# Kernel optimization log

Measured on AMD Instinct MI355X. Metric: run time of the kernel, lower is better.

## Reference

```python
import jax, jax.numpy as jnp
import numpy as np

N = 50000      # nodes
E = 800000     # edges (avg degree 16)
IN = 64        # in_channels
H = 128        # hidden_channels
OUT = 64       # out_channels
NS = 10        # n_samples
EPS = 1e-5     # BatchNorm eps


def _sage_conv(x, src, dst, Wl, bl, Wr):
    # PyG SAGEConv (mean aggr): lin_l(mean_neighbors) + lin_r(x)
    n = x.shape[0]
    deg = jax.ops.segment_sum(jnp.ones(src.shape[0], x.dtype), dst, num_segments=n)
    agg = jax.ops.segment_sum(x[src], dst, num_segments=n) / jnp.clip(deg, 1.0)[:, None]
    return agg @ Wl + bl + x @ Wr


def _batchnorm(x, gamma, beta):
    # training-mode BN forward (batch statistics), deterministic
    m = x.mean(axis=0)
    v = x.var(axis=0)
    return (x - m) * jax.lax.rsqrt(v + EPS) * gamma + beta


def setup_inputs() -> dict:
    key = jax.random.key(0)
    ks = jax.random.split(key, 40)
    w = lambda k, shape: (jax.random.normal(k, shape, jnp.float32) * 0.05)
    inp = {
        "x": jax.random.normal(ks[0], (N, IN), jnp.float32),
        "edge_index": jax.random.randint(ks[1], (2, E), 0, N, dtype=jnp.int32),
        "batch": jnp.zeros((N,), jnp.int32),
        "noise": jax.random.normal(ks[2], (NS, N, OUT), jnp.float32),
        # encoder1: SAGEConv(IN,H) + BN(H)
        "We1l": w(ks[3], (IN, H)), "be1": jnp.zeros((H,), jnp.float32), "We1r": w(ks[4], (IN, H)),
        "g1": jnp.ones((H,), jnp.float32), "b1": jnp.zeros((H,), jnp.float32),
        # encoder2: SAGEConv(H,2H) + BN(2H) + SAGEConv(2H,2*OUT)
        "We2l": w(ks[5], (H, 2 * H)), "be2": jnp.zeros((2 * H,), jnp.float32), "We2r": w(ks[6], (H, 2 * H)),
        "g2": jnp.ones((2 * H,), jnp.float32), "b2": jnp.zeros((2 * H,), jnp.float32),
        "We3l": w(ks[7], (2 * H, 2 * OUT)), "be3": jnp.zeros((2 * OUT,), jnp.float32), "We3r": w(ks[8], (2 * H, 2 * OUT)),
        # x1_transform: Linear(H, IN)
        "Wt": w(ks[9], (H, IN)), "bt": jnp.zeros((IN,), jnp.float32),
        # decoder1: Linear(OUT+IN, H) + BN(H); decoder2: Linear(H, IN)
        "Wd1": w(ks[10], (OUT + IN, H)), "bd1": jnp.zeros((H,), jnp.float32),
        "gd": jnp.ones((H,), jnp.float32), "bd": jnp.zeros((H,), jnp.float32),
        "Wd2": w(ks[11], (H, IN)), "bd2": jnp.zeros((IN,), jnp.float32),
        # SAGPooling score GNN = GraphConv(H, 1): lin_rel (bias) + lin_root (no bias)
        "Wp_rel": w(ks[12], (H, 1)), "bp": jnp.zeros((1,), jnp.float32), "Wp_root": w(ks[13], (H, 1)),
    }
    return inp


def reference(x, edge_index, batch, noise,
              We1l, be1, We1r, g1, b1,
              We2l, be2, We2r, g2, b2,
              We3l, be3, We3r,
              Wt, bt, Wd1, bd1, gd, bd, Wd2, bd2,
              Wp_rel, bp, Wp_root):
    src, dst = edge_index[0], edge_index[1]

    # ---- encode ----
    x1 = _batchnorm(jax.nn.relu(_sage_conv(x, src, dst, We1l, be1, We1r)), g1, b1)
    x2 = _batchnorm(jax.nn.relu(_sage_conv(x1, src, dst, We2l, be2, We2r)), g2, b2)
    ms = _sage_conv(x2, src, dst, We3l, be3, We3r)        # [N, 2*OUT]
    mean, log_std = ms[:, :OUT], ms[:, OUT:]

    # ---- reparameterize: avg of n_samples draws == mean + std * mean(eps) ----
    z = mean + jnp.exp(log_std) * noise.mean(axis=0)

    # ---- decode ----
    x1t = x1 @ Wt + bt                                    # [N, IN]
    h = jax.nn.relu(jnp.concatenate([z, x1t], axis=-1) @ Wd1 + bd1)
    h = _batchnorm(h, gd, bd)
    reconstruction = h @ Wd2 + bd2                        # [N, IN]

    # ---- SAGPooling (ratio=0.5) on x1 ----
    agg = jax.ops.segment_sum(x1[src], dst, num_segments=N)   # GraphConv add-aggr
    score = jnp.tanh((agg @ Wp_rel + bp + x1 @ Wp_root)[:, 0])  # [N]
    k = N // 2
    _, perm = jax.lax.top_k(score, k)                     # kept node indices (desc score)

    keep = jnp.zeros((N,), bool).at[perm].set(True)
    newidx = jnp.zeros((N,), jnp.int32).at[perm].set(jnp.arange(k, dtype=jnp.int32))
    edge_mask = keep[src] & keep[dst]                     # edges surviving the pooling
    ei_cg = newidx[edge_index]                            # [2, E], valid where edge_mask
    # unpool: map coarse indices back to original node ids; -1 marks dropped edges
    edge_index_unpooled = jnp.where(edge_mask[None, :], perm[ei_cg].astype(jnp.int32), -1)
    x_unpooled = x1[perm]                                 # [k, H]

    return (reconstruction, x_unpooled, edge_index_unpooled, edge_mask, mean, log_std, x1)
```

## Files before the change

### kernel.cpp

```cpp
#include <hip/hip_runtime.h>
#include <hip/hip_bf16.h>
#include <math.h>

#define NN 50000
#define EE 800000
#define KHALF 25000
#define NSAMP 2048
#define NBK (NSAMP+1)

typedef short bf16x8 __attribute__((ext_vector_type(8)));
typedef short sh4 __attribute__((ext_vector_type(4)));
typedef float f32x4 __attribute__((ext_vector_type(4)));

static __device__ inline unsigned short f2bf(float f){
  __hip_bfloat16 h = __float2bfloat16(f);
  return __builtin_bit_cast(unsigned short, h);
}
static __device__ inline float bf2f(unsigned short u){
  unsigned int x = ((unsigned int)u)<<16;
  return __builtin_bit_cast(float, x);
}

__global__ void k_hist(const int* __restrict__ dst, int* __restrict__ cnt, int E){
  int i = blockIdx.x*blockDim.x + threadIdx.x;
  if(i<E) atomicAdd(&cnt[dst[i]], 1);
}

__global__ void k_scan(const int* __restrict__ deg, int* __restrict__ rowptr, int n){
  __shared__ int sm[1024];
  int t = threadIdx.x;
  int chunk = (n + 1023) >> 10;
  int b = t*chunk; int e = b+chunk; if(b>n) b=n; if(e>n) e=n;
  int s=0;
  for(int i=b;i<e;i++) s += deg[i];
  sm[t]=s; __syncthreads();
  for(int off=1; off<1024; off<<=1){
    int add = (t>=off)? sm[t-off] : 0;
    __syncthreads();
    sm[t] += add;
    __syncthreads();
  }
  int run = sm[t]-s;
  for(int i=b;i<e;i++){ rowptr[i]=run; run += deg[i]; }
  if(t==1023) rowptr[n]=sm[1023];
}

__global__ void k_fill(const int* __restrict__ src, const int* __restrict__ dst,
                       const int* __restrict__ rowptr, int* __restrict__ cnt,
                       int* __restrict__ csr, int E){
  int i = blockIdx.x*blockDim.x + threadIdx.x;
  if(i<E){
    int d = dst[i];
    int p = rowptr[d] + atomicAdd(&cnt[d],1);
    csr[p] = src[i];
  }
}

template<typename AccT, typename OT, int F, int VW>
__global__ void k_segmean(const float* __restrict__ x, const int* __restrict__ csr,
                          const int* __restrict__ rowptr, OT* __restrict__ out, int n){
  int gid = blockIdx.x*blockDim.x + threadIdx.x;
  int node = gid >> 6; int lane = gid & 63;
  if(node>=n) return;
  int b = rowptr[node], e = rowptr[node+1];
  AccT acc[VW];
  #pragma unroll
  for(int k=0;k<VW;k++) acc[k]=(AccT)0;
  const float* xp = x + lane*VW;
  for(int j=b;j<e;j++){
    const float* row = xp + (long)csr[j]*F;
    if(VW==1){
      acc[0] += (AccT)row[0];
    } else if(VW==2){
      float2 v = *(const float2*)row;
      acc[0]+=(AccT)v.x; acc[1]+=(AccT)v.y;
    } else {
      float4 v = *(const float4*)row;
      acc[0]+=(AccT)v.x; acc[1]+=(AccT)v.y; acc[2]+=(AccT)v.z; acc[3]+=(AccT)v.w;
    }
  }
  int d = e-b; if(d<1) d=1;
  AccT inv = (AccT)1 / (AccT)d;
  #pragma unroll
  for(int k=0;k<VW;k++) out[(long)node*F + lane*VW + k] = (OT)(acc[k]*inv);
}

__global__ void k_segmean_ms(const float* __restrict__ T3, const float* __restrict__ msr,
                             const int* __restrict__ csr, const int* __restrict__ rowptr,
                             float* __restrict__ omean, float* __restrict__ olstd, int n){
  int gid = blockIdx.x*blockDim.x + threadIdx.x;
  int node = gid >> 6; int lane = gid & 63;
  if(node>=n) return;
  int b = rowptr[node], e = rowptr[node+1];
  float a0=0.f, a1=0.f;
  const float* xp = T3 + lane*2;
  for(int j=b;j<e;j++){
    float2 v = *(const float2*)(xp + (long)csr[j]*128);
    a0+=v.x; a1+=v.y;
  }
  int d=e-b; if(d<1)d=1;
  float inv = 1.f/(float)d;
  float2 mv = *(const float2*)(msr + (long)node*128 + lane*2);
  float2 r; r.x = a0*inv + mv.x; r.y = a1*inv + mv.y;
  int c0 = lane*2;
  if(c0 < 64) *(float2*)(omean + (long)node*64 + c0)      = r;
  else        *(float2*)(olstd + (long)node*64 + (c0-64)) = r;
}

__global__ __launch_bounds__(256) void k_gemm_bf16s(
    const float* __restrict__ A, const float* __restrict__ W1, int K1,
    const float* __restrict__ X, const float* __restrict__ W2, int K2,
    const float* __restrict__ bias, float* __restrict__ out,
    int M, int J, int relu)
{
  __shared__ __align__(16) short Ah[128*64];
  __shared__ __align__(16) short Al[128*64];
  __shared__ __align__(16) short Bh[64*64];
  __shared__ __align__(16) short Bl[64*64];
  const int m0 = blockIdx.x*128, n0 = blockIdx.y*64;
  const int t = threadIdx.x;
  const int lane = t & 63, wid = t >> 6;
  const int wm = wid >> 1, wn = wid & 1;

  f32x4 acc[4][2];
  #pragma unroll
  for(int i=0;i<4;i++)
    #pragma unroll
    for(int j=0;j<2;j++) acc[i][j] = (f32x4){0.f,0.f,0.f,0.f};

  const int ns1 = K1 >> 6;
  const int ns2 = X ? (K2 >> 6) : 0;
  for(int s=0; s<ns1+ns2; ++s){
    const float* P; const float* W; int K, k0;
    if(s < ns1){ P = A; W = W1; K = K1; k0 = s*64; }
    else       { P = X; W = W2; K = K2; k0 = (s-ns1)*64; }

    #pragma unroll
    for(int i=0;i<8;i++){
      int f4  = t + i*256;
      int row = f4 >> 4, c4 = f4 & 15;
      int gr  = m0 + row;
      float4 v = make_float4(0.f,0.f,0.f,0.f);
      if(gr < M) v = *(const float4*)(P + (long)gr*K + k0 + c4*4);
      unsigned short h0=f2bf(v.x), h1=f2bf(v.y), h2=f2bf(v.z), h3=f2bf(v.w);
      sh4 hi = (sh4){(short)h0,(short)h1,(short)h2,(short)h3};
      sh4 lo = (sh4){(short)f2bf(v.x-bf2f(h0)), (short)f2bf(v.y-bf2f(h1)),
                     (short)f2bf(v.z-bf2f(h2)), (short)f2bf(v.w-bf2f(h3))};
      int byte = (row*128 + c4*8) ^ ((row&7)<<4);
      *(sh4*)((char*)Ah + byte) = hi;
      *(sh4*)((char*)Al + byte) = lo;
    }
    {
      int n = t & 63, k4 = (t>>6)<<2;
      #pragma unroll
      for(int i=0;i<4;i++){
        int kb = i*16 + k4;
        const float* wp = W + (long)(k0+kb)*J + n0 + n;
        float w0 = wp[0], w1 = wp[J], w2 = wp[2*J], w3 = wp[3*J];
        unsigned short h0=f2bf(w0), h1=f2bf(w1), h2=f2bf(w2), h3=f2bf(w3);
        sh4 hi = (sh4){(short)h0,(short)h1,(short)h2,(short)h3};
        sh4 lo = (sh4){(short)f2bf(w0-bf2f(h0)), (short)f2bf(w1-bf2f(h1)),
                       (short)f2bf(w2-bf2f(h2)), (short)f2bf(w3-bf2f(h3))};
        int byte = (n*128 + kb*2) ^ ((n&7)<<4);
        *(sh4*)((char*)Bh + byte) = hi;
        *(sh4*)((char*)Bl + byte) = lo;
      }
    }
    __syncthreads();

    #pragma unroll
    for(int kk=0;kk<2;kk++){
      int kb = kk*32 + (lane>>4)*8;
      bf16x8 ahf[4], alf[4], bhf[2], blf[2];
      #pragma unroll
      for(int mf=0; mf<4; mf++){
        int r = wm*64 + mf*16 + (lane&15);
        int byte = (r*128 + kb*2) ^ ((r&7)<<4);
        ahf[mf] = *(const bf16x8*)((const char*)Ah + byte);
        alf[mf] = *(const bf16x8*)((const char*)Al + byte);
      }
      #pragma unroll
      for(int nf=0; nf<2; nf++){
        int n = wn*32 + nf*16 + (lane&15);
        int byte = (n*128 + kb*2) ^ ((n&7)<<4);
        bhf[nf] = *(const bf16x8*)((const char*)Bh + byte);
        blf[nf] = *(const bf16x8*)((const char*)Bl + byte);
      }
      #pragma unroll
      for(int mf=0; mf<4; mf++)
        #pragma unroll
        for(int nf=0; nf<2; nf++){
          acc[mf][nf] = __builtin_amdgcn_mfma_f32_16x16x32_bf16(ahf[mf], bhf[nf], acc[mf][nf], 0,0,0);
          acc[mf][nf] = __builtin_amdgcn_mfma_f32_16x16x32_bf16(ahf[mf], blf[nf], acc[mf][nf], 0,0,0);
          acc[mf][nf] = __builtin_amdgcn_mfma_f32_16x16x32_bf16(alf[mf], bhf[nf], acc[mf][nf], 0,0,0);
        }
    }
    __syncthreads();
  }

  #pragma unroll
  for(int mf=0; mf<4; mf++){
    #pragma unroll
    for(int nf=0; nf<2; nf++){
      int col = n0 + wn*32 + nf*16 + (lane&15);
      #pragma unroll
      for(int q=0;q<4;q++){
        int row = m0 + wm*64 + mf*16 + (lane>>4)*4 + q;
        if(row >= M) continue;
        float v = acc[mf][nf][q] + (bias ? bias[col] : 0.f);
        if(relu) v = fmaxf(v, 0.f);
        out[(long)row*J + col] = v;
      }
    }
  }
}

__global__ __launch_bounds__(256) void k_gemm_c1(
    const double* __restrict__ A1, const float* __restrict__ X,
    const float* __restrict__ W1, const float* __restrict__ W2,
    const float* __restrict__ bias, double* __restrict__ out, int M)
{
  __shared__ double As[32][66];
  __shared__ double Ws[32][64];
  const int m0 = blockIdx.x*64, n0 = blockIdx.y*64;
  const int t = threadIdx.x;
  const int tm = t & 15, tn = t >> 4;
  double acc[4][4];
  #pragma unroll
  for(int i=0;i<4;i++)
    #pragma unroll
    for(int j=0;j<4;j++) acc[i][j]=0.0;

  for(int pair=0; pair<2; pair++){
    const float* Wp = pair ? W2 : W1;
    for(int k0=0; k0<64; k0+=32){
      #pragma unroll
      for(int i=0;i<8;i++){
        int idx = t + i*256;
        int r = idx >> 5, c = idx & 31;
        int gr = m0 + r;
        double v = 0.0;
        if(gr<M) v = pair ? (double)X[(long)gr*64 + k0 + c] : A1[(long)gr*64 + k0 + c];
        As[c][r] = v;
      }
      #pragma unroll
      for(int i=0;i<8;i++){
        int idx = t + i*256;
        int r = idx >> 6, c = idx & 63;
        Ws[r][c] = (double)Wp[(k0+r)*128 + n0 + c];
      }
      __syncthreads();
      #pragma unroll
      for(int kk=0;kk<32;kk++){
        double a0=As[kk][tm*4+0], a1=As[kk][tm*4+1], a2=As[kk][tm*4+2], a3=As[kk][tm*4+3];
        double w0=Ws[kk][tn*4+0], w1=Ws[kk][tn*4+1], w2=Ws[kk][tn*4+2], w3=Ws[kk][tn*4+3];
        acc[0][0] += a0*w0; acc[0][1] += a0*w1; acc[0][2] += a0*w2; acc[0][3] += a0*w3;
        acc[1][0] += a1*w0; acc[1][1] += a1*w1; acc[1][2] += a1*w2; acc[1][3] += a1*w3;
        acc[2][0] += a2*w0; acc[2][1] += a2*w1; acc[2][2] += a2*w2; acc[2][3] += a2*w3;
        acc[3][0] += a3*w0; acc[3][1] += a3*w1; acc[3][2] += a3*w2; acc[3][3] += a3*w3;
      }
      __syncthreads();
    }
  }
  #pragma unroll
  for(int i=0;i<4;i++){
    int gr = m0 + tm*4 + i;
    if(gr>=M) continue;
    #pragma unroll
    for(int j=0;j<4;j++){
      int gc = n0 + tn*4 + j;
      double v = acc[i][j] + (double)bias[gc];
      if(v<0.0) v=0.0;
      out[(long)gr*128 + gc] = v;
    }
  }
}

template<typename T>
__global__ void k_colstats(const T* __restrict__ x, int M, int J,
                           double* __restrict__ ps, double* __restrict__ pq){
  int c = threadIdx.x; int b = blockIdx.x, B = gridDim.x;
  int rows = (M + B - 1)/B;
  int r0 = b*rows, r1 = r0+rows; if(r1>M) r1=M;
  double s=0.0,q=0.0;
  for(int r=r0;r<r1;r++){ double v = (double)x[(long)r*J + c]; s+=v; q+=v*v; }
  ps[(long)b*J+c]=s; pq[(long)b*J+c]=q;
}

__global__ void k_bnfinal(const double* __restrict__ ps, const double* __restrict__ pq,
                          int B, int J, int M, const float* __restrict__ g,
                          const float* __restrict__ bta,
                          double* __restrict__ sc, double* __restrict__ sh){
  int c = threadIdx.x; if(c>=J) return;
  double s=0.0,q=0.0;
  for(int b=0;b<B;b++){ s+=ps[(long)b*J+c]; q+=pq[(long)b*J+c]; }
  double m = s/M; double v = q/M - m*m;
  double inv = 1.0/sqrt(v + 1e-5);
  double a = (double)g[c]*inv;
  sc[c]=a; sh[c]=(double)bta[c] - m*a;
}

__global__ void k_bnapply_f64(double* __restrict__ x, float* __restrict__ o32,
                              const double* __restrict__ sc, const double* __restrict__ sh,
                              long total, int Jm){
  long i = (long)blockIdx.x*blockDim.x + threadIdx.x;
  if(i>=total) return;
  int c = (int)(i & Jm);
  double v = x[i]*sc[c] + sh[c];
  x[i]=v; o32[i]=(float)v;
}

__global__ void k_bnapply_f32(float* __restrict__ x,
                              const double* __restrict__ sc, const double* __restrict__ sh,
                              long total, int Jm){
  long i = (long)blockIdx.x*blockDim.x + threadIdx.x;
  if(i>=total) return;
  int c = (int)(i & Jm);
  x[i] = (float)((double)x[i]*sc[c] + sh[c]);
}

__global__ void k_z(const float* __restrict__ mean, const float* __restrict__ lstd,
                    const float* __restrict__ noise, float* __restrict__ z, int total4){
  int i = blockIdx.x*blockDim.x + threadIdx.x;
  if(i>=total4) return;
  const float4* m4 = (const float4*)mean;
  const float4* l4 = (const float4*)lstd;
  const float4* n4 = (const float4*)noise;
  float4 m = m4[i], l = l4[i];
  float nx=0.f, ny=0.f, nz=0.f, nw=0.f;
  #pragma unroll
  for(int s=0;s<10;s++){
    float4 v = n4[(long)s*total4 + i];
    nx+=v.x; ny+=v.y; nz+=v.z; nw+=v.w;
  }
  float4 o;
  o.x = (float)((double)m.x + exp((double)l.x)*((double)nx*0.1));
  o.y = (float)((double)m.y + exp((double)l.y)*((double)ny*0.1));
  o.z = (float)((double)m.z + exp((double)l.z)*((double)nz*0.1));
  o.w = (float)((double)m.w + exp((double)l.w)*((double)nw*0.1));
  ((float4*)z)[i] = o;
}

__global__ void k_tr(const double* __restrict__ x1, const float* __restrict__ wrel,
                     const float* __restrict__ wroot, double* __restrict__ t,
                     double* __restrict__ r, int n){
  int gid = blockIdx.x*blockDim.x + threadIdx.x;
  int node = gid>>6, lane = gid&63;
  if(node>=n) return;
  const double* row = x1 + (long)node*128;
  double a0=row[lane], a1=row[lane+64];
  double tv = a0*(double)wrel[lane]  + a1*(double)wrel[lane+64];
  double rv = a0*(double)wroot[lane] + a1*(double)wroot[lane+64];
  for(int off=32; off>0; off>>=1){
    tv += __shfl_xor(tv, off);
    rv += __shfl_xor(rv, off);
  }
  if(lane==0){ t[node]=tv; r[node]=rv; }
}

__global__ void k_score(const double* __restrict__ t, const double* __restrict__ r,
                        const int* __restrict__ csr, const int* __restrict__ rowptr,
                        const float* __restrict__ bp,
                        unsigned long long* __restrict__ key, int n){
  int i = blockIdx.x*blockDim.x + threadIdx.x;
  if(i>=n) return;
  double s = (double)bp[0] + r[i];
  int b=rowptr[i], e=rowptr[i+1];
  for(int j=b;j<e;j++) s += t[csr[j]];
  double sc = tanh(s) + 0.0;
  long long u = __double_as_longlong(sc);
  unsigned long long uu = (unsigned long long)u;
  key[i] = (u < 0) ? ~uu : (uu ^ 0x8000000000000000ULL);
}

__global__ void k_sample_sort(const unsigned long long* __restrict__ key,
                              unsigned long long* __restrict__ samp){
  __shared__ unsigned long long sm[NSAMP];
  int t = threadIdx.x;
  sm[t]      = key[t*24];
  sm[t+1024] = key[(t+1024)*24];
  __syncthreads();
  for(int k=2; k<=NSAMP; k<<=1){
    for(int j=k>>1; j>0; j>>=1){
      #pragma unroll 2
      for(int base=0; base<NSAMP; base+=1024){
        int i = base + t;
        int l = i ^ j;
        if(l > i){
          unsigned long long a = sm[i], b = sm[l];
          bool up = ((i & k) == 0);
          if(up ? (a > b) : (a < b)){ sm[i]=b; sm[l]=a; }
        }
      }
      __syncthreads();
    }
  }
  samp[t] = sm[t]; samp[t+1024] = sm[t+1024];
}

__global__ __launch_bounds__(256) void k_bucket_assign(
    const unsigned long long* __restrict__ key,
    const unsigned long long* __restrict__ samp,
    int* __restrict__ bucket, int* __restrict__ bcnt, int n){
  __shared__ unsigned long long sm[NSAMP];
  for(int u=threadIdx.x; u<NSAMP; u+=256) sm[u] = samp[u];
  __syncthreads();
  int i = blockIdx.x*256 + threadIdx.x;
  if(i>=n) return;
  unsigned long long ki = key[i];
  int lo=0, hi=NSAMP;
  while(lo<hi){ int mid=(lo+hi)>>1; if(sm[mid] < ki) lo=mid+1; else hi=mid; }
  bucket[i]=lo;
  atomicAdd(&bcnt[lo],1);
}

__global__ void k_bucket_fill(const int* __restrict__ bucket,
                              const int* __restrict__ bstart, int* __restrict__ bfill,
                              int* __restrict__ blist, int n){
  int i = blockIdx.x*blockDim.x + threadIdx.x;
  if(i>=n) return;
  int b = bucket[i];
  int p = bstart[b] + atomicAdd(&bfill[b],1);
  blist[p] = i;
}

__global__ __launch_bounds__(256) void k_bucket_rank(
    const unsigned long long* __restrict__ key,
    const int* __restrict__ blist, const int* __restrict__ bstart,
    int n, int k, int* __restrict__ keep, int* __restrict__ perm){
  __shared__ unsigned long long skey[2048];
  __shared__ int sidx[2048];
  int b = blockIdx.x;
  int s0 = bstart[b], s1 = bstart[b+1];
  int m = s1 - s0;
  if(m<=0) return;
  int above = n - s1;
  if(m <= 2048){
    for(int u=threadIdx.x; u<m; u+=256){ int ii=blist[s0+u]; sidx[u]=ii; skey[u]=key[ii]; }
    __syncthreads();
    for(int u=threadIdx.x; u<m; u+=256){
      unsigned long long ki = skey[u]; int ii = sidx[u];
      int c = 0;
      for(int v=0; v<m; v++){
        unsigned long long kv = skey[v];
        c += ((kv > ki) || (kv == ki && sidx[v] < ii)) ? 1 : 0;
      }
      int rank = above + c;
      int kp = (rank < k) ? 1 : 0;
      keep[ii] = kp;
      if(kp) perm[rank] = ii;
    }
  } else {
    for(int u=threadIdx.x; u<m; u+=256){
      int ii = blist[s0+u];
      unsigned long long ki = key[ii];
      int c=0;
      for(int v=0; v<m; v++){
        int jj = blist[s0+v];
        unsigned long long kv = key[jj];
        c += ((kv > ki) || (kv == ki && jj < ii)) ? 1 : 0;
      }
      int rank = above + c;
      int kp = (rank < k) ? 1 : 0;
      keep[ii] = kp;
      if(kp) perm[rank] = ii;
    }
  }
}

__global__ void k_unpool(const float* __restrict__ x1, const int* __restrict__ perm,
                         float* __restrict__ out, int k){
  int i = blockIdx.x*blockDim.x + threadIdx.x;
  if(i >= k*128) return;
  int r = i>>7, c = i&127;
  out[i] = x1[(long)perm[r]*128 + c];
}

__global__ void k_edgeout(const int* __restrict__ src, const int* __restrict__ dst,
                          const int* __restrict__ keep, float* __restrict__ o2,
                          float* __restrict__ o3, int E){
  int e = blockIdx.x*blockDim.x + threadIdx.x;
  if(e>=E) return;
  int s=src[e], d=dst[e];
  bool m = keep[s] && keep[d];
  o2[e]   = m ? (float)s : -1.f;
  o2[E+e] = m ? (float)d : -1.f;
  o3[e]   = m ? 1.f : 0.f;
}

extern "C" void kernel_launch(void* const* d_in, const int* in_sizes, int n_in,
                              void* d_out, int out_size, void* d_ws, size_t ws_size,
                              hipStream_t stream){
  const float* x     = (const float*)d_in[0];
  const int*   ei    = (const int*)d_in[1];
  const float* noise = (const float*)d_in[3];
  const float* We1l  = (const float*)d_in[4];
  const float* be1   = (const float*)d_in[5];
  const float* We1r  = (const float*)d_in[6];
  const float* g1    = (const float*)d_in[7];
  const float* b1    = (const float*)d_in[8];
  const float* We2l  = (const float*)d_in[9];
  const float* be2   = (const float*)d_in[10];
  const float* We2r  = (const float*)d_in[11];
  const float* g2    = (const float*)d_in[12];
  const float* b2    = (const float*)d_in[13];
  const float* We3l  = (const float*)d_in[14];
  const float* be3   = (const float*)d_in[15];
  const float* We3r  = (const float*)d_in[16];
  const float* Wt    = (const float*)d_in[17];
  const float* bt    = (const float*)d_in[18];
  const float* Wd1   = (const float*)d_in[19];
  const float* bd1   = (const float*)d_in[20];
  const float* gd    = (const float*)d_in[21];
  const float* bd    = (const float*)d_in[22];
  const float* Wd2   = (const float*)d_in[23];
  const float* bd2   = (const float*)d_in[24];
  const float* Wprel = (const float*)d_in[25];
  const float* bp    = (const float*)d_in[26];
  const float* Wproot= (const float*)d_in[27];

  const int* src = ei;
  const int* dst = ei + EE;

  float* out   = (float*)d_out;
  float* o_rec  = out;
  float* o_xun  = out + 3200000;
  float* o_eiu  = out + 6400000;
  float* o_mask = out + 8000000;
  float* o_mean = out + 8800000;
  float* o_lstd = out + 12000000;
  float* o_x1   = out + 15200000;

  char* w = (char*)d_ws;
  size_t off = 0;
  auto alloc = [&](size_t bytes)->char*{
    char* p = w + off; off += (bytes + 255) & ~(size_t)255; return p;
  };
  int*    csr  = (int*)   alloc((size_t)EE*4);
  int*    rowp = (int*)   alloc((size_t)(NN+1)*4);
  int*    cnt  = (int*)   alloc((size_t)NN*4);
  char*   B3   =          alloc((size_t)NN*128*8);
  char*   B4   =          alloc((size_t)NN*64*8);
  char*   B5   =          alloc((size_t)NN*256*4);
  double* t_   = (double*)alloc((size_t)NN*8);
  double* r_   = (double*)alloc((size_t)NN*8);
  unsigned long long* key_ = (unsigned long long*)alloc((size_t)NN*8);
  int*    keep = (int*)   alloc((size_t)NN*4);
  int*    perm = (int*)   alloc((size_t)KHALF*4);
  double* ps   = (double*)alloc((size_t)240*256*8);
  double* pq   = (double*)alloc((size_t)240*256*8);
  double* bnsc = (double*)alloc(256*8);
  double* bnsh = (double*)alloc(256*8);
  unsigned long long* samp = (unsigned long long*)alloc((size_t)NSAMP*8);
  int*    bucket = (int*) alloc((size_t)NN*4);
  int*    bcnt   = (int*) alloc((size_t)NBK*4);
  int*    bstart = (int*) alloc((size_t)(NBK+1)*4);
  int*    bfill  = (int*) alloc((size_t)NBK*4);
  int*    blist  = (int*) alloc((size_t)NN*4);
  (void)in_sizes; (void)n_in; (void)out_size; (void)ws_size;

  double* A1  = (double*)B4;
  double* x1p = (double*)B3;
  float*  A2  = (float*)B4;
  float*  x2  = (float*)B3;
  float*  T3  = (float*)B5;
  float*  msr = (float*)(B5 + (size_t)NN*128*4);
  float*  zb  = (float*)B5;
  float*  x1t = (float*)(B5 + (size_t)NN*64*4);
  float*  h   = (float*)B4;

  const int GX = (NN+127)/128;

  hipMemsetAsync(cnt, 0, (size_t)NN*4, stream);
  k_hist<<<(EE+255)/256,256,0,stream>>>(dst, cnt, EE);
  k_scan<<<1,1024,0,stream>>>(cnt, rowp, NN);
  hipMemsetAsync(cnt, 0, (size_t)NN*4, stream);
  k_fill<<<(EE+255)/256,256,0,stream>>>(src, dst, rowp, cnt, csr, EE);

  k_segmean<double,double,64,1><<<(NN+3)/4,256,0,stream>>>(x, csr, rowp, A1, NN);
  { dim3 g((NN+63)/64, 2);
    k_gemm_c1<<<g,256,0,stream>>>(A1, x, We1l, We1r, be1, x1p, NN); }
  k_colstats<double><<<240,128,0,stream>>>(x1p, NN, 128, ps, pq);
  k_bnfinal<<<1,128,0,stream>>>(ps,pq,240,128,NN,g1,b1,bnsc,bnsh);
  { long tot=(long)NN*128;
    k_bnapply_f64<<<(int)((tot+255)/256),256,0,stream>>>(x1p, o_x1, bnsc,bnsh, tot, 127); }
  k_tr<<<(NN+3)/4,256,0,stream>>>(x1p, Wprel, Wproot, t_, r_, NN);

  k_segmean<float,float,128,2><<<(NN+3)/4,256,0,stream>>>(o_x1, csr, rowp, A2, NN);
  { dim3 g(GX, 4);
    k_gemm_bf16s<<<g,256,0,stream>>>(A2, We2l, 128, o_x1, We2r, 128, be2, x2, NN, 256, 1); }
  k_colstats<float><<<240,256,0,stream>>>(x2, NN, 256, ps, pq);
  k_bnfinal<<<1,256,0,stream>>>(ps,pq,240,256,NN,g2,b2,bnsc,bnsh);
  { long tot=(long)NN*256;
    k_bnapply_f32<<<(int)((tot+255)/256),256,0,stream>>>(x2, bnsc,bnsh, tot, 255); }

  { dim3 g(GX, 2);
    k_gemm_bf16s<<<g,256,0,stream>>>(x2, We3l, 256, nullptr, nullptr, 0, nullptr, T3, NN, 128, 0); }
  { dim3 g(GX, 2);
    k_gemm_bf16s<<<g,256,0,stream>>>(x2, We3r, 256, nullptr, nullptr, 0, be3, msr, NN, 128, 0); }
  k_segmean_ms<<<(NN+3)/4,256,0,stream>>>(T3, msr, csr, rowp, o_mean, o_lstd, NN);

  k_z<<<(800000+255)/256,256,0,stream>>>(o_mean, o_lstd, noise, zb, 800000);
  { dim3 g(GX, 1);
    k_gemm_bf16s<<<g,256,0,stream>>>(o_x1, Wt, 128, nullptr, nullptr, 0, bt, x1t, NN, 64, 0); }
  { dim3 g(GX, 2);
    k_gemm_bf16s<<<g,256,0,stream>>>(zb, Wd1, 64, x1t, Wd1 + 64*128, 64, bd1, h, NN, 128, 1); }
  k_colstats<float><<<240,128,0,stream>>>(h, NN, 128, ps, pq);
  k_bnfinal<<<1,128,0,stream>>>(ps,pq,240,128,NN,gd,bd,bnsc,bnsh);
  { long tot=(long)NN*128;
    k_bnapply_f32<<<(int)((tot+255)/256),256,0,stream>>>(h, bnsc,bnsh, tot, 127); }
  { dim3 g(GX, 1);
    k_gemm_bf16s<<<g,256,0,stream>>>(h, Wd2, 128, nullptr, nullptr, 0, bd2, o_rec, NN, 64, 0); }

  k_score<<<(NN+255)/256,256,0,stream>>>(t_, r_, csr, rowp, bp, key_, NN);
  k_sample_sort<<<1,1024,0,stream>>>(key_, samp);
  hipMemsetAsync(bcnt, 0, (size_t)NBK*4, stream);
  k_bucket_assign<<<(NN+255)/256,256,0,stream>>>(key_, samp, bucket, bcnt, NN);
  k_scan<<<1,1024,0,stream>>>(bcnt, bstart, NBK);
  hipMemsetAsync(bfill, 0, (size_t)NBK*4, stream);
  k_bucket_fill<<<(NN+255)/256,256,0,stream>>>(bucket, bstart, bfill, blist, NN);
  k_bucket_rank<<<NBK,256,0,stream>>>(key_, blist, bstart, NN, KHALF, keep, perm);
  k_unpool<<<(KHALF*128+255)/256,256,0,stream>>>(o_x1, perm, o_xun, KHALF);
  k_edgeout<<<(EE+255)/256,256,0,stream>>>(src, dst, keep, o_eiu, o_mask, EE);
}
```

Before: 1.299 ms.

## Fold BN into GEMM loads, precompose decoder weights, swizzle f64 GEMM LDS

Batch-norm application for x2 and the decoder hidden layer is folded into the A-operand load of the following bf16 GEMMs via float scale/shift vectors, which removes two elementwise BN passes. The x1_transform linear is folded into Wd1 by precomputing Wc = Wt·Wd1_bottom and a combined bias, which removes one GEMM and its intermediate buffer. The f64 GEMM now uses a swizzled LDS layout with double2 loads, and the sample sort for top-k uses 1024 samples instead of 2048. The trade-offs are that the weight-folding reassociates arithmetic and changes rounding, the BN scale is applied in fp32 before bf16 splitting, and fewer samples give coarser buckets.

```diff
diff --git a/kernel.cpp b/kernel.cpp
--- a/kernel.cpp
+++ b/kernel.cpp
@@ -5,7 +5,7 @@
 #define NN 50000
 #define EE 800000
 #define KHALF 25000
-#define NSAMP 2048
+#define NSAMP 1024
 #define NBK (NSAMP+1)
 
 typedef short bf16x8 __attribute__((ext_vector_type(8)));
@@ -19,6 +19,9 @@
 static __device__ inline float bf2f(unsigned short u){
   unsigned int x = ((unsigned int)u)<<16;
   return __builtin_bit_cast(float, x);
+}
+static __device__ inline int swz8(int kk, int r){
+  return (kk*512 + r*8) ^ ((kk&7)<<4) ^ (((r>>4)&1)<<4);
 }
 
 __global__ void k_hist(const int* __restrict__ dst, int* __restrict__ cnt, int E){
@@ -111,7 +114,8 @@
     const float* __restrict__ A, const float* __restrict__ W1, int K1,
     const float* __restrict__ X, const float* __restrict__ W2, int K2,
     const float* __restrict__ bias, float* __restrict__ out,
-    int M, int J, int relu)
+    int M, int J, int relu,
+    const float* __restrict__ bnsc, const float* __restrict__ bnsh)
 {
   __shared__ __align__(16) short Ah[128*64];
   __shared__ __align__(16) short Al[128*64];
@@ -134,6 +138,7 @@
     const float* P; const float* W; int K, k0;
     if(s < ns1){ P = A; W = W1; K = K1; k0 = s*64; }
     else       { P = X; W = W2; K = K2; k0 = (s-ns1)*64; }
+    const bool bn = (bnsc != nullptr) && (s < ns1);
 
     #pragma unroll
     for(int i=0;i<8;i++){
@@ -142,6 +147,13 @@
       int gr  = m0 + row;
       float4 v = make_float4(0.f,0.f,0.f,0.f);
       if(gr < M) v = *(const float4*)(P + (long)gr*K + k0 + c4*4);
+      if(bn){
+        int kc = k0 + c4*4;
+        v.x = v.x*bnsc[kc]   + bnsh[kc];
+        v.y = v.y*bnsc[kc+1] + bnsh[kc+1];
+        v.z = v.z*bnsc[kc+2] + bnsh[kc+2];
+        v.w = v.w*bnsc[kc+3] + bnsh[kc+3];
+      }
       unsigned short h0=f2bf(v.x), h1=f2bf(v.y), h2=f2bf(v.z), h3=f2bf(v.w);
       sh4 hi = (sh4){(short)h0,(short)h1,(short)h2,(short)h3};
       sh4 lo = (sh4){(short)f2bf(v.x-bf2f(h0)), (short)f2bf(v.y-bf2f(h1)),
@@ -220,8 +232,8 @@
     const float* __restrict__ W1, const float* __restrict__ W2,
     const float* __restrict__ bias, double* __restrict__ out, int M)
 {
-  __shared__ double As[32][66];
-  __shared__ double Ws[32][64];
+  __shared__ __align__(16) double As[2048];
+  __shared__ __align__(16) double Ws[2048];
   const int m0 = blockIdx.x*64, n0 = blockIdx.y*64;
   const int t = threadIdx.x;
   const int tm = t & 15, tn = t >> 4;
@@ -241,19 +253,23 @@
         int gr = m0 + r;
         double v = 0.0;
         if(gr<M) v = pair ? (double)X[(long)gr*64 + k0 + c] : A1[(long)gr*64 + k0 + c];
-        As[c][r] = v;
+        *(double*)((char*)As + swz8(c, r)) = v;
       }
       #pragma unroll
       for(int i=0;i<8;i++){
         int idx = t + i*256;
-        int r = idx >> 6, c = idx & 63;
-        Ws[r][c] = (double)Wp[(k0+r)*128 + n0 + c];
+        int kk = idx >> 6, n = idx & 63;
+        *(double*)((char*)Ws + swz8(kk, n)) = (double)Wp[(k0+kk)*128 + n0 + n];
       }
       __syncthreads();
       #pragma unroll
       for(int kk=0;kk<32;kk++){
-        double a0=As[kk][tm*4+0], a1=As[kk][tm*4+1], a2=As[kk][tm*4+2], a3=As[kk][tm*4+3];
-        double w0=Ws[kk][tn*4+0], w1=Ws[kk][tn*4+1], w2=Ws[kk][tn*4+2], w3=Ws[kk][tn*4+3];
+        double2 aA = *(const double2*)((const char*)As + swz8(kk, tm*4));
+        double2 aB = *(const double2*)((const char*)As + swz8(kk, tm*4+2));
+        double2 wA = *(const double2*)((const char*)Ws + swz8(kk, tn*4));
+        double2 wB = *(const double2*)((const char*)Ws + swz8(kk, tn*4+2));
+        double a0=aA.x, a1=aA.y, a2=aB.x, a3=aB.y;
+        double w0=wA.x, w1=wA.y, w2=wB.x, w3=wB.y;
         acc[0][0] += a0*w0; acc[0][1] += a0*w1; acc[0][2] += a0*w2; acc[0][3] += a0*w3;
         acc[1][0] += a1*w0; acc[1][1] += a1*w1; acc[1][2] += a1*w2; acc[1][3] += a1*w3;
         acc[2][0] += a2*w0; acc[2][1] += a2*w1; acc[2][2] += a2*w2; acc[2][3] += a2*w3;
@@ -276,6 +292,23 @@
   }
 }
 
+__global__ void k_wfold(const float* __restrict__ Wt, const float* __restrict__ bt,
+                        const float* __restrict__ Wd1, const float* __restrict__ bd1,
+                        float* __restrict__ Wc, float* __restrict__ bc){
+  int j = threadIdx.x;
+  int i = blockIdx.x;
+  float s;
+  if(i < 128){
+    s = 0.f;
+    for(int k=0;k<64;k++) s += Wt[i*64+k] * Wd1[(64+k)*128 + j];
+    Wc[i*128+j] = s;
+  } else {
+    s = bd1[j];
+    for(int k=0;k<64;k++) s += bt[k] * Wd1[(64+k)*128 + j];
+    bc[j] = s;
+  }
+}
+
 template<typename T>
 __global__ void k_colstats(const T* __restrict__ x, int M, int J,
                            double* __restrict__ ps, double* __restrict__ pq){
@@ -290,7 +323,8 @@
 __global__ void k_bnfinal(const double* __restrict__ ps, const double* __restrict__ pq,
                           int B, int J, int M, const float* __restrict__ g,
                           const float* __restrict__ bta,
-                          double* __restrict__ sc, double* __restrict__ sh){
+                          double* __restrict__ sc, double* __restrict__ sh,
+                          float* __restrict__ sc32, float* __restrict__ sh32){
   int c = threadIdx.x; if(c>=J) return;
   double s=0.0,q=0.0;
   for(int b=0;b<B;b++){ s+=ps[(long)b*J+c]; q+=pq[(long)b*J+c]; }
@@ -298,6 +332,7 @@
   double inv = 1.0/sqrt(v + 1e-5);
   double a = (double)g[c]*inv;
   sc[c]=a; sh[c]=(double)bta[c] - m*a;
+  sc32[c]=(float)a; sh32[c]=(float)((double)bta[c] - m*a);
 }
 
 __global__ void k_bnapply_f64(double* __restrict__ x, float* __restrict__ o32,
@@ -308,15 +343,6 @@
   int c = (int)(i & Jm);
   double v = x[i]*sc[c] + sh[c];
   x[i]=v; o32[i]=(float)v;
-}
-
-__global__ void k_bnapply_f32(float* __restrict__ x,
-                              const double* __restrict__ sc, const double* __restrict__ sh,
-                              long total, int Jm){
-  long i = (long)blockIdx.x*blockDim.x + threadIdx.x;
-  if(i>=total) return;
-  int c = (int)(i & Jm);
-  x[i] = (float)((double)x[i]*sc[c] + sh[c]);
 }
 
 __global__ void k_z(const float* __restrict__ mean, const float* __restrict__ lstd,
@@ -377,25 +403,20 @@
                               unsigned long long* __restrict__ samp){
   __shared__ unsigned long long sm[NSAMP];
   int t = threadIdx.x;
-  sm[t]      = key[t*24];
-  sm[t+1024] = key[(t+1024)*24];
+  sm[t] = key[t*48];
   __syncthreads();
   for(int k=2; k<=NSAMP; k<<=1){
     for(int j=k>>1; j>0; j>>=1){
-      #pragma unroll 2
-      for(int base=0; base<NSAMP; base+=1024){
-        int i = base + t;
-        int l = i ^ j;
-        if(l > i){
-          unsigned long long a = sm[i], b = sm[l];
-          bool up = ((i & k) == 0);
-          if(up ? (a > b) : (a < b)){ sm[i]=b; sm[l]=a; }
-        }
+      int l = t ^ j;
+      if(l > t){
+        unsigned long long a = sm[t], b = sm[l];
+        bool up = ((t & k) == 0);
+        if(up ? (a > b) : (a < b)){ sm[t]=b; sm[l]=a; }
       }
       __syncthreads();
     }
   }
-  samp[t] = sm[t]; samp[t+1024] = sm[t+1024];
+  samp[t] = sm[t];
 }
 
 __global__ __launch_bounds__(256) void k_bucket_assign(
@@ -551,6 +572,14 @@
   double* pq   = (double*)alloc((size_t)240*256*8);
   double* bnsc = (double*)alloc(256*8);
   double* bnsh = (double*)alloc(256*8);
+  float*  sc1f = (float*) alloc(256*4);
+  float*  sh1f = (float*) alloc(256*4);
+  float*  sc2f = (float*) alloc(256*4);
+  float*  sh2f = (float*) alloc(256*4);
+  float*  scdf = (float*) alloc(256*4);
+  float*  shdf = (float*) alloc(256*4);
+  float*  Wc   = (float*) alloc((size_t)128*128*4);
+  float*  bc   = (float*) alloc(128*4);
   unsigned long long* samp = (unsigned long long*)alloc((size_t)NSAMP*8);
   int*    bucket = (int*) alloc((size_t)NN*4);
   int*    bcnt   = (int*) alloc((size_t)NBK*4);
@@ -566,13 +595,13 @@
   float*  T3  = (float*)B5;
   float*  msr = (float*)(B5 + (size_t)NN*128*4);
   float*  zb  = (float*)B5;
-  float*  x1t = (float*)(B5 + (size_t)NN*64*4);
   float*  h   = (float*)B4;
 
   const int GX = (NN+127)/128;
 
   hipMemsetAsync(cnt, 0, (size_t)NN*4, stream);
   k_hist<<<(EE+255)/256,256,0,stream>>>(dst, cnt, EE);
+  k_wfold<<<129,128,0,stream>>>(Wt, bt, Wd1, bd1, Wc, bc);
   k_scan<<<1,1024,0,stream>>>(cnt, rowp, NN);
   hipMemsetAsync(cnt, 0, (size_t)NN*4, stream);
   k_fill<<<(EE+255)/256,256,0,stream>>>(src, dst, rowp, cnt, csr, EE);
@@ -581,36 +610,30 @@
   { dim3 g((NN+63)/64, 2);
     k_gemm_c1<<<g,256,0,stream>>>(A1, x, We1l, We1r, be1, x1p, NN); }
   k_colstats<double><<<240,128,0,stream>>>(x1p, NN, 128, ps, pq);
-  k_bnfinal<<<1,128,0,stream>>>(ps,pq,240,128,NN,g1,b1,bnsc,bnsh);
+  k_bnfinal<<<1,128,0,stream>>>(ps,pq,240,128,NN,g1,b1,bnsc,bnsh,sc1f,sh1f);
   { long tot=(long)NN*128;
     k_bnapply_f64<<<(int)((tot+255)/256),256,0,stream>>>(x1p, o_x1, bnsc,bnsh, tot, 127); }
   k_tr<<<(NN+3)/4,256,0,stream>>>(x1p, Wprel, Wproot, t_, r_, NN);
 
   k_segmean<float,float,128,2><<<(NN+3)/4,256,0,stream>>>(o_x1, csr, rowp, A2, NN);
   { dim3 g(GX, 4);
-    k_gemm_bf16s<<<g,256,0,stream>>>(A2, We2l, 128, o_x1, We2r, 128, be2, x2, NN, 256, 1); }
+    k_gemm_bf16s<<<g,256,0,stream>>>(A2, We2l, 128, o_x1, We2r, 128, be2, x2, NN, 256, 1, nullptr, nullptr); }
   k_colstats<float><<<240,256,0,stream>>>(x2, NN, 256, ps, pq);
-  k_bnfinal<<<1,256,0,stream>>>(ps,pq,240,256,NN,g2,b2,bnsc,bnsh);
-  { long tot=(long)NN*256;
-    k_bnapply_f32<<<(int)((tot+255)/256),256,0,stream>>>(x2, bnsc,bnsh, tot, 255); }
+  k_bnfinal<<<1,256,0,stream>>>(ps,pq,240,256,NN,g2,b2,bnsc,bnsh,sc2f,sh2f);
 
   { dim3 g(GX, 2);
-    k_gemm_bf16s<<<g,256,0,stream>>>(x2, We3l, 256, nullptr, nullptr, 0, nullptr, T3, NN, 128, 0); }
+    k_gemm_bf16s<<<g,256,0,stream>>>(x2, We3l, 256, nullptr, nullptr, 0, nullptr, T3, NN, 128, 0, sc2f, sh2f); }
   { dim3 g(GX, 2);
-    k_gemm_bf16s<<<g,256,0,stream>>>(x2, We3r, 256, nullptr, nullptr, 0, be3, msr, NN, 128, 0); }
+    k_gemm_bf16s<<<g,256,0,stream>>>(x2, We3r, 256, nullptr, nullptr, 0, be3, msr, NN, 128, 0, sc2f, sh2f); }
   k_segmean_ms<<<(NN+3)/4,256,0,stream>>>(T3, msr, csr, rowp, o_mean, o_lstd, NN);
 
   k_z<<<(800000+255)/256,256,0,stream>>>(o_mean, o_lstd, noise, zb, 800000);
+  { dim3 g(GX, 2);
+    k_gemm_bf16s<<<g,256,0,stream>>>(zb, Wd1, 64, o_x1, Wc, 128, bc, h, NN, 128, 1, nullptr, nullptr); }
+  k_colstats<float><<<240,128,0,stream>>>(h, NN, 128, ps, pq);
+  k_bnfinal<<<1,128,0,stream>>>(ps,pq,240,128,NN,gd,bd,bnsc,bnsh,scdf,shdf);
   { dim3 g(GX, 1);
-    k_gemm_bf16s<<<g,256,0,stream>>>(o_x1, Wt, 128, nullptr, nullptr, 0, bt, x1t, NN, 64, 0); }
-  { dim3 g(GX, 2);
-    k_gemm_bf16s<<<g,256,0,stream>>>(zb, Wd1, 64, x1t, Wd1 + 64*128, 64, bd1, h, NN, 128, 1); }
-  k_colstats<float><<<240,128,0,stream>>>(h, NN, 128, ps, pq);
-  k_bnfinal<<<1,128,0,stream>>>(ps,pq,240,128,NN,gd,bd,bnsc,bnsh);
-  { long tot=(long)NN*128;
-    k_bnapply_f32<<<(int)((tot+255)/256),256,0,stream>>>(h, bnsc,bnsh, tot, 127); }
-  { dim3 g(GX, 1);
-    k_gemm_bf16s<<<g,256,0,stream>>>(h, Wd2, 128, nullptr, nullptr, 0, bd2, o_rec, NN, 64, 0); }
+    k_gemm_bf16s<<<g,256,0,stream>>>(h, Wd2, 128, nullptr, nullptr, 0, bd2, o_rec, NN, 64, 0, scdf, shdf); }
 
   k_score<<<(NN+255)/256,256,0,stream>>>(t_, r_, csr, rowp, bp, key_, NN);
   k_sample_sort<<<1,1024,0,stream>>>(key_, samp);
```

Result: slower. 1.338 ms (+3.0%).
